# Kernel tuning notes

Measured on AMD Instinct MI355X. Metric: run time of the kernel, lower is better.

The kernel has to match this reference:

```python
import jax, jax.numpy as jnp
import numpy as np

N, E, D_IN, H, DH = 50000, 800000, 128, 4, 32
NEG_SLOPE = 0.01  # torch nn.LeakyReLU() default
EPS = 1e-16       # torch_geometric softmax epsilon


def setup_inputs() -> dict:
    key = jax.random.key(0)
    k0, k1, k2, k3, k4 = jax.random.split(key, 5)
    x = jax.random.normal(k0, (N, D_IN), dtype=jnp.float32)
    edge_index = jax.random.randint(k1, (2, E), 0, N, dtype=jnp.int64)
    # Glorot-uniform-ish scales
    s_proj = (6.0 / (D_IN + H * DH)) ** 0.5
    W_proj = jax.random.uniform(k2, (D_IN, H * DH), jnp.float32, -s_proj, s_proj)
    s_att = (6.0 / (H + 2 * DH)) ** 0.5
    att_w = jax.random.uniform(k3, (H, 2 * DH), jnp.float32, -s_att, s_att)
    W_skip = jax.random.uniform(k4, (D_IN, H * DH), jnp.float32, -s_proj, s_proj)
    return {"x": x, "W_proj": W_proj, "att_w": att_w, "W_skip": W_skip,
            "edge_index": edge_index}


def reference(x, W_proj, att_w, W_skip, edge_index):
    num_nodes = x.shape[0]
    h = (x @ W_proj).reshape(num_nodes, H, DH)          # [N,H,Dh]
    src, dst = edge_index[0], edge_index[1]
    h_src = h[src]                                      # [E,H,Dh] gather
    h_dst = h[dst]                                      # [E,H,Dh] gather
    # einsum('nah,nah->na', cat([h_src,h_dst],-1), a) == split-a form:
    a_src, a_dst = att_w[:, :DH], att_w[:, DH:]
    e = (jnp.einsum('ehd,hd->eh', h_src, a_src)
         + jnp.einsum('ehd,hd->eh', h_dst, a_dst))      # [E,H]
    e = jax.nn.leaky_relu(e, NEG_SLOPE)
    # segment softmax grouped by dst (max-stabilized, as in torch_geometric)
    e_max = jax.ops.segment_max(e, dst, num_segments=num_nodes)  # [N,H]
    e_exp = jnp.exp(e - e_max[dst])
    denom = jax.ops.segment_sum(e_exp, dst, num_segments=num_nodes)
    alpha = e_exp / (denom[dst] + EPS)                  # [E,H]
    # scatter-add aggregation (index_add_ by dst)
    h_prime = jax.ops.segment_sum(alpha[..., None] * h_src, dst,
                                  num_segments=num_nodes)  # [N,H,Dh]
    h_prime = h_prime + (x @ W_skip).reshape(num_nodes, H, DH)
    return h_prime.reshape(num_nodes, H * DH)
```

## Files before the change

kernel.cpp:

```cpp
#include <hip/hip_runtime.h>
#include <hip/hip_bf16.h>

#define N_NODES 50000
#define E_EDGES 800000
#define NHEAD 4
#define DHEAD 32
#define DOUT 128
#define NEG_SLOPE 0.01f
#define EPS_F 1e-16f
#define DMAX 256
#define ELP 264
#define NB 196
#define CAP 8192

typedef __attribute__((ext_vector_type(8))) short bf16x8;
typedef __attribute__((ext_vector_type(4))) float f32x4;

__device__ __forceinline__ float bf2f(unsigned short u) {
    return __uint_as_float((unsigned)u << 16);
}
__device__ __forceinline__ unsigned short f2bf(float f) {
    return __bfloat16_as_ushort(__float2bfloat16(f));
}

__device__ __forceinline__ void load_edge(const int* __restrict__ ei, int isI64,
                                          int e, int& src, int& dst) {
    if (isI64) { src = ei[2 * e]; dst = ei[2 * (E_EDGES + e)]; }
    else       { src = ei[e];     dst = ei[E_EDGES + e]; }
}

__global__ __launch_bounds__(128) void k_prep(const float* __restrict__ Wp,
                                              const float* __restrict__ Ws,
                                              const int* __restrict__ ei,
                                              unsigned short* __restrict__ Wt,
                                              int* __restrict__ flag) {
    int b = blockIdx.x;
    if (b < 256) {
        int c = b, k = threadIdx.x;
        float v = (c < DOUT) ? Wp[k * DOUT + c] : Ws[k * DOUT + (c - DOUT)];
        int nf = c >> 4, cl = c & 15;
        int ks = k >> 5, r = k & 31, lq = r >> 3, e = r & 7;
        Wt[(((nf * 4 + ks) << 6) + lq * 16 + cl) * 8 + e] = f2bf(v);
    } else {
        __shared__ int cnt;
        if (threadIdx.x == 0) cnt = 0;
        __syncthreads();
        int nz = 0;
        #pragma unroll
        for (int k2 = 0; k2 < 16; ++k2) {
            int pos = (threadIdx.x + k2 * 128) * 2 + 1;
            if (ei[pos] != 0) nz = 1;
        }
        if (nz) atomicOr(&cnt, 1);
        __syncthreads();
        if (threadIdx.x == 0) *flag = (cnt == 0) ? 1 : 0;
    }
}

#define HBP 136
#define SKP 132
__global__ __launch_bounds__(256) void k_gemm(const float* __restrict__ x,
                                              const unsigned short* __restrict__ Wt,
                                              const float* __restrict__ att,
                                              unsigned short* __restrict__ hb,
                                              float* __restrict__ as_,
                                              float* __restrict__ ad_,
                                              float* __restrict__ out) {
    __shared__ float SK[64 * SKP];
    __shared__ unsigned short HB[64 * HBP];
    char* XSc = (char*)SK;

    const int tid = threadIdx.x;
    const int rw  = tid >> 6;
    const int l   = tid & 63;
    const int l15 = l & 15;
    const int lq  = l >> 4;

    {
        int d = tid * 16;
        #pragma unroll
        for (int it = 0; it < 8; ++it, d += 4096) {
            int row = d >> 9, col = d & 511;
            int grow = blockIdx.x * 64 + row;
            if (grow > N_NODES - 1) grow = N_NODES - 1;
            float4 v = *(const float4*)((const char*)x + (size_t)grow * 512 + col);
            *(float4*)(XSc + (row << 9) + (col ^ ((row & 7) << 4))) = v;
        }
    }
    __syncthreads();

    const int rl = rw * 16 + l15;
    const int sw = (rl & 7) << 4;
    bf16x8 afr[4];
    #pragma unroll
    for (int ks = 0; ks < 4; ++ks) {
        int c0 = ks * 128 + lq * 32;
        float4 u0 = *(const float4*)(XSc + (rl << 9) + (c0 ^ sw));
        float4 u1 = *(const float4*)(XSc + (rl << 9) + ((c0 + 16) ^ sw));
        bf16x8 a;
        a[0] = (short)f2bf(u0.x); a[1] = (short)f2bf(u0.y);
        a[2] = (short)f2bf(u0.z); a[3] = (short)f2bf(u0.w);
        a[4] = (short)f2bf(u1.x); a[5] = (short)f2bf(u1.y);
        a[6] = (short)f2bf(u1.z); a[7] = (short)f2bf(u1.w);
        afr[ks] = a;
    }
    __syncthreads();

    f32x4 acc[16];
    #pragma unroll
    for (int nf = 0; nf < 16; ++nf) acc[nf] = (f32x4)(0.0f);

    #pragma unroll
    for (int nf = 0; nf < 16; ++nf) {
        #pragma unroll
        for (int ks = 0; ks < 4; ++ks) {
            bf16x8 b = *(const bf16x8*)(Wt + ((((nf * 4 + ks) << 6) + l) << 3));
            acc[nf] = __builtin_amdgcn_mfma_f32_16x16x32_bf16(afr[ks], b, acc[nf], 0, 0, 0);
        }
    }

    #pragma unroll
    for (int nf = 0; nf < 8; ++nf) {
        #pragma unroll
        for (int q = 0; q < 4; ++q) {
            int r2 = rw * 16 + lq * 4 + q;
            HB[r2 * HBP + nf * 16 + l15] = f2bf(acc[nf][q]);
        }
    }
    #pragma unroll
    for (int nf = 8; nf < 16; ++nf) {
        #pragma unroll
        for (int q = 0; q < 4; ++q) {
            int r2 = rw * 16 + lq * 4 + q;
            SK[r2 * SKP + (nf - 8) * 16 + l15] = acc[nf][q];
        }
    }
    __syncthreads();

    {
        int rl2 = tid >> 2, hd = tid & 3;
        const unsigned* HBu = (const unsigned*)HB;
        const float* a1 = att + hd * 2 * DHEAD;
        const float* a2 = a1 + DHEAD;
        float s1 = 0.0f, s2 = 0.0f;
        #pragma unroll
        for (int j = 0; j < 16; ++j) {
            unsigned u = HBu[rl2 * (HBP / 2) + hd * 16 + j];
            float lo = bf2f((unsigned short)(u & 0xffff));
            float hi = bf2f((unsigned short)(u >> 16));
            s1 += lo * a1[2 * j] + hi * a1[2 * j + 1];
            s2 += lo * a2[2 * j] + hi * a2[2 * j + 1];
        }
        int rowg = blockIdx.x * 64 + rl2;
        as_[(size_t)rowg * 4 + hd] = s1;
        ad_[(size_t)rowg * 4 + hd] = s2;
    }

    {
        const unsigned* HBu = (const unsigned*)HB;
        #pragma unroll
        for (int it = 0; it < 4; ++it) {
            int idx = it * 256 + tid;
            int row = idx >> 4, g = idx & 15;
            int wb = row * (HBP / 2) + g * 4;
            uint4 v;
            v.x = HBu[wb]; v.y = HBu[wb + 1]; v.z = HBu[wb + 2]; v.w = HBu[wb + 3];
            *(uint4*)(hb + ((size_t)(blockIdx.x * 64 + row)) * DOUT + g * 8) = v;
        }
    }
    {
        #pragma unroll
        for (int it = 0; it < 8; ++it) {
            int idx = it * 256 + tid;
            int row = idx >> 5, c4 = idx & 31;
            int rowg = blockIdx.x * 64 + row;
            if (rowg < N_NODES) {
                float4 v = *(const float4*)&SK[row * SKP + c4 * 4];
                *(float4*)(out + (size_t)rowg * DOUT + c4 * 4) = v;
            }
        }
    }
}

__global__ __launch_bounds__(256) void k_part(const int* __restrict__ ei,
                                              const int* __restrict__ flag,
                                              int* __restrict__ bucketCnt,
                                              unsigned* __restrict__ payload) {
    __shared__ int hist[NB];
    __shared__ int curs[NB];
    const int t = threadIdx.x;
    const int base = blockIdx.x * 3125;
    const int isI64 = *flag;

    for (int i = t; i < NB; i += 256) hist[i] = 0;
    __syncthreads();
    for (int i = t; i < 3125; i += 256) {
        int src, dst;
        load_edge(ei, isI64, base + i, src, dst);
        if ((unsigned)dst < N_NODES) atomicAdd(&hist[dst >> 8], 1);
    }
    __syncthreads();
    for (int i = t; i < NB; i += 256)
        curs[i] = atomicAdd(&bucketCnt[i], hist[i]);
    __syncthreads();
    for (int i = t; i < 3125; i += 256) {
        int src, dst;
        load_edge(ei, isI64, base + i, src, dst);
        if ((unsigned)src >= N_NODES || (unsigned)dst >= N_NODES) continue;
        int b = dst >> 8;
        int pos = atomicAdd(&curs[b], 1);
        if (pos < CAP)
            payload[((size_t)b << 13) + pos] = ((unsigned)(dst & 255) << 16) | (unsigned)src;
    }
}

__global__ __launch_bounds__(256) void k_csr(const int* __restrict__ bucketCnt,
                                             const unsigned* __restrict__ payload,
                                             int* __restrict__ deg,
                                             int* __restrict__ ofs,
                                             int* __restrict__ srcs) {
    __shared__ int h[256];
    __shared__ int cur[256];
    __shared__ int sc[256];
    const int b = blockIdx.x;
    const int t = threadIdx.x;
    int cnt = bucketCnt[b];
    if (cnt > CAP) cnt = CAP;
    const unsigned* __restrict__ pl = payload + ((size_t)b << 13);

    h[t] = 0;
    __syncthreads();
    for (int i = t; i < cnt; i += 256) atomicAdd(&h[pl[i] >> 16], 1);
    __syncthreads();
    int v = h[t];
    sc[t] = v;
    __syncthreads();
    #pragma unroll
    for (int off = 1; off < 256; off <<= 1) {
        int u = (t >= off) ? sc[t - off] : 0;
        __syncthreads();
        sc[t] += u;
        __syncthreads();
    }
    int ex = sc[t] - v;
    cur[t] = ex;
    int n = (b << 8) + t;
    if (n < N_NODES) { deg[n] = v; ofs[n] = (b << 13) + ex; }
    __syncthreads();
    for (int i = t; i < cnt; i += 256) {
        unsigned p = pl[i];
        int pos = atomicAdd(&cur[p >> 16], 1);
        srcs[((size_t)b << 13) + pos] = (int)(p & 0xFFFFu);
    }
}

__global__ __launch_bounds__(128) void k_gat(const int* __restrict__ ofs,
                                             const int* __restrict__ deg,
                                             const int* __restrict__ srcs,
                                             const float* __restrict__ as_,
                                             const float* __restrict__ ad_,
                                             const unsigned short* __restrict__ hb,
                                             float* __restrict__ out) {
    __shared__ float EL[2][NHEAD * ELP];
    __shared__ int   SRC[2][DMAX];

    const int sub = threadIdx.x >> 6;
    const int k   = threadIdx.x & 63;
    const int hd  = k >> 4;
    const int l16 = k & 15;
    const int n = blockIdx.x * 2 + sub;
    const int o = ofs[n];
    const int d = deg[n];
    const unsigned* __restrict__ hbu = (const unsigned*)hb;
    float* ELn = EL[sub];
    int*   SRCn = SRC[sub];

    int fast = __syncthreads_and(d <= DMAX);

    if (fast) {
        const float4 adv4 = *(const float4*)(ad_ + (size_t)n * 4);
        for (int e = k; e < d; e += 64) {
            int s = srcs[o + e];
            SRCn[e] = s;
            float4 a4 = *(const float4*)(as_ + (size_t)s * 4);
            float e0 = a4.x + adv4.x, e1 = a4.y + adv4.y;
            float e2 = a4.z + adv4.z, e3 = a4.w + adv4.w;
            ELn[0 * ELP + e] = (e0 > 0.0f) ? e0 : NEG_SLOPE * e0;
            ELn[1 * ELP + e] = (e1 > 0.0f) ? e1 : NEG_SLOPE * e1;
            ELn[2 * ELP + e] = (e2 > 0.0f) ? e2 : NEG_SLOPE * e2;
            ELn[3 * ELP + e] = (e3 > 0.0f) ? e3 : NEG_SLOPE * e3;
        }
        __syncthreads();
        float m = -3.4e38f;
        for (int i = l16; i < d; i += 16) m = fmaxf(m, ELn[hd * ELP + i]);
        #pragma unroll
        for (int off = 8; off; off >>= 1) m = fmaxf(m, __shfl_xor(m, off));
        float den = 0.0f;
        for (int i = l16; i < d; i += 16) {
            float p = __expf(ELn[hd * ELP + i] - m);
            ELn[hd * ELP + i] = p;
            den += p;
        }
        #pragma unroll
        for (int off = 8; off; off >>= 1) den += __shfl_xor(den, off);
        __syncthreads();
        float num0 = 0.0f, num1 = 0.0f;
        int i = 0;
        for (; i + 4 <= d; i += 4) {
            int s0 = SRCn[i], s1 = SRCn[i + 1], s2 = SRCn[i + 2], s3 = SRCn[i + 3];
            unsigned u0 = hbu[(size_t)s0 * (DOUT / 2) + k];
            unsigned u1 = hbu[(size_t)s1 * (DOUT / 2) + k];
            unsigned u2 = hbu[(size_t)s2 * (DOUT / 2) + k];
            unsigned u3 = hbu[(size_t)s3 * (DOUT / 2) + k];
            float p0 = ELn[hd * ELP + i];
            float p1 = ELn[hd * ELP + i + 1];
            float p2 = ELn[hd * ELP + i + 2];
            float p3 = ELn[hd * ELP + i + 3];
            num0 = fmaf(p0, bf2f((unsigned short)(u0 & 0xffff)), num0);
            num1 = fmaf(p0, bf2f((unsigned short)(u0 >> 16)), num1);
            num0 = fmaf(p1, bf2f((unsigned short)(u1 & 0xffff)), num0);
            num1 = fmaf(p1, bf2f((unsigned short)(u1 >> 16)), num1);
            num0 = fmaf(p2, bf2f((unsigned short)(u2 & 0xffff)), num0);
            num1 = fmaf(p2, bf2f((unsigned short)(u2 >> 16)), num1);
            num0 = fmaf(p3, bf2f((unsigned short)(u3 & 0xffff)), num0);
            num1 = fmaf(p3, bf2f((unsigned short)(u3 >> 16)), num1);
        }
        for (; i < d; ++i) {
            float p = ELn[hd * ELP + i];
            int s = SRCn[i];
            unsigned u = hbu[(size_t)s * (DOUT / 2) + k];
            num0 = fmaf(p, bf2f((unsigned short)(u & 0xffff)), num0);
            num1 = fmaf(p, bf2f((unsigned short)(u >> 16)), num1);
        }
        float inv = 1.0f / (den + EPS_F);
        float2* op = (float2*)(out + (size_t)n * DOUT + 2 * k);
        float2 sk = *op;
        *op = make_float2(num0 * inv + sk.x, num1 * inv + sk.y);
    } else {
        const float adv = ad_[(size_t)n * 4 + hd];
        float m = -3.4e38f;
        for (int i = 0; i < d; ++i) {
            float el = as_[(size_t)srcs[o + i] * 4 + hd] + adv;
            el = (el > 0.0f) ? el : NEG_SLOPE * el;
            m = fmaxf(m, el);
        }
        float den = 0.0f, num0 = 0.0f, num1 = 0.0f;
        for (int i = 0; i < d; ++i) {
            int s = srcs[o + i];
            float el = as_[(size_t)s * 4 + hd] + adv;
            el = (el > 0.0f) ? el : NEG_SLOPE * el;
            float p = __expf(el - m);
            den += p;
            unsigned u = hbu[(size_t)s * (DOUT / 2) + k];
            num0 = fmaf(p, bf2f((unsigned short)(u & 0xffff)), num0);
            num1 = fmaf(p, bf2f((unsigned short)(u >> 16)), num1);
        }
        float inv = 1.0f / (den + EPS_F);
        float2* op = (float2*)(out + (size_t)n * DOUT + 2 * k);
        float2 sk = *op;
        *op = make_float2(num0 * inv + sk.x, num1 * inv + sk.y);
    }
}

extern "C" void kernel_launch(void* const* d_in, const int* in_sizes, int n_in,
                              void* d_out, int out_size, void* d_ws, size_t ws_size,
                              hipStream_t stream) {
    const float* x   = (const float*)d_in[0];
    const float* Wp  = (const float*)d_in[1];
    const float* att = (const float*)d_in[2];
    const float* Ws  = (const float*)d_in[3];
    const int*   ei  = (const int*)d_in[4];
    float* out = (float*)d_out;

    char* ws = (char*)d_ws;
    unsigned short* hb        = (unsigned short*)(ws);
    unsigned short* Wt        = (unsigned short*)(ws + 12812288);
    float*          as_       = (float*)(ws + 12877824);
    float*          ad_       = (float*)(ws + 13678592);
    int*            deg       = (int*)(ws + 14479360);
    int*            ofs       = (int*)(ws + 14680064);
    unsigned*       payload   = (unsigned*)(ws + 14880768);
    int*            srcs      = (int*)(ws + 21303296);
    int*            bucketCnt = (int*)(ws + 27725824);
    int*            flag      = (int*)(ws + 27726848);

    hipMemsetAsync(bucketCnt, 0, NB * 4, stream);

    k_prep<<<257, 128, 0, stream>>>(Wp, Ws, ei, Wt, flag);
    k_gemm<<<(N_NODES + 63) / 64, 256, 0, stream>>>(x, Wt, att, hb, as_, ad_, out);
    k_part<<<256, 256, 0, stream>>>(ei, flag, bucketCnt, payload);
    k_csr<<<NB, 256, 0, stream>>>(bucketCnt, payload, deg, ofs, srcs);
    k_gat<<<N_NODES / 2, 128, 0, stream>>>(ofs, deg, srcs, as_, ad_, hb, out);
}
```

Measured before the change: 118.2 us.

## Merge edge partition into GEMM launch and store GEMM outputs directly from registers

The edge bucketing kernel and the projection GEMM now run as one launch: the first 256 blocks do the partition and the rest do the GEMM, so the two independent stages can overlap and one launch is removed. The GEMM converts x to bf16 while staging it into shared memory and swaps the MFMA operand order so each lane holds a row's outputs. The attention dot products are then computed straight from the accumulators with shuffle reductions, and hb and out are written directly without a shared-memory round trip. This trades fewer barriers and less shared-memory traffic for scattered 8-byte and 16-byte global stores and a mixed-workload grid.

```diff
diff --git a/kernel.cpp b/kernel.cpp
--- a/kernel.cpp
+++ b/kernel.cpp
@@ -12,6 +12,7 @@
 #define ELP 264
 #define NB 196
 #define CAP 8192
+#define XSP 136
 
 typedef __attribute__((ext_vector_type(8))) short bf16x8;
 typedef __attribute__((ext_vector_type(4))) float f32x4;
@@ -57,54 +58,76 @@
     }
 }
 
-#define HBP 136
-#define SKP 132
-__global__ __launch_bounds__(256) void k_gemm(const float* __restrict__ x,
-                                              const unsigned short* __restrict__ Wt,
-                                              const float* __restrict__ att,
-                                              unsigned short* __restrict__ hb,
-                                              float* __restrict__ as_,
-                                              float* __restrict__ ad_,
-                                              float* __restrict__ out) {
-    __shared__ float SK[64 * SKP];
-    __shared__ unsigned short HB[64 * HBP];
-    char* XSc = (char*)SK;
-
+__global__ __launch_bounds__(256) void k_gemm_part(const float* __restrict__ x,
+                                                   const unsigned short* __restrict__ Wt,
+                                                   const float* __restrict__ att,
+                                                   const int* __restrict__ ei,
+                                                   const int* __restrict__ flag,
+                                                   int* __restrict__ bucketCnt,
+                                                   unsigned* __restrict__ payload,
+                                                   unsigned short* __restrict__ hb,
+                                                   float* __restrict__ as_,
+                                                   float* __restrict__ ad_,
+                                                   float* __restrict__ out) {
+    __shared__ __align__(16) char BUF[64 * XSP * 2];
     const int tid = threadIdx.x;
+
+    if (blockIdx.x < 256) {
+        int* hist = (int*)BUF;
+        int* curs = hist + NB;
+        const int base = blockIdx.x * 3125;
+        const int isI64 = *flag;
+
+        for (int i = tid; i < NB; i += 256) hist[i] = 0;
+        __syncthreads();
+        for (int i = tid; i < 3125; i += 256) {
+            int src, dst;
+            load_edge(ei, isI64, base + i, src, dst);
+            if ((unsigned)dst < N_NODES) atomicAdd(&hist[dst >> 8], 1);
+        }
+        __syncthreads();
+        for (int i = tid; i < NB; i += 256)
+            curs[i] = atomicAdd(&bucketCnt[i], hist[i]);
+        __syncthreads();
+        for (int i = tid; i < 3125; i += 256) {
+            int src, dst;
+            load_edge(ei, isI64, base + i, src, dst);
+            if ((unsigned)src >= N_NODES || (unsigned)dst >= N_NODES) continue;
+            int b = dst >> 8;
+            int pos = atomicAdd(&curs[b], 1);
+            if (pos < CAP)
+                payload[((size_t)b << 13) + pos] = ((unsigned)(dst & 255) << 16) | (unsigned)src;
+        }
+        return;
+    }
+
+    unsigned short* XSB = (unsigned short*)BUF;
+    const int gb  = blockIdx.x - 256;
     const int rw  = tid >> 6;
     const int l   = tid & 63;
     const int l15 = l & 15;
     const int lq  = l >> 4;
+    const int rowbase = gb * 64 + rw * 16;
 
     {
-        int d = tid * 16;
-        #pragma unroll
-        for (int it = 0; it < 8; ++it, d += 4096) {
-            int row = d >> 9, col = d & 511;
-            int grow = blockIdx.x * 64 + row;
+        #pragma unroll
+        for (int it = 0; it < 8; ++it) {
+            int e = it * 1024 + tid * 4;
+            int row = e >> 7, col = e & 127;
+            int grow = gb * 64 + row;
             if (grow > N_NODES - 1) grow = N_NODES - 1;
-            float4 v = *(const float4*)((const char*)x + (size_t)grow * 512 + col);
-            *(float4*)(XSc + (row << 9) + (col ^ ((row & 7) << 4))) = v;
-        }
-    }
-    __syncthreads();
-
-    const int rl = rw * 16 + l15;
-    const int sw = (rl & 7) << 4;
-    bf16x8 afr[4];
-    #pragma unroll
-    for (int ks = 0; ks < 4; ++ks) {
-        int c0 = ks * 128 + lq * 32;
-        float4 u0 = *(const float4*)(XSc + (rl << 9) + (c0 ^ sw));
-        float4 u1 = *(const float4*)(XSc + (rl << 9) + ((c0 + 16) ^ sw));
-        bf16x8 a;
-        a[0] = (short)f2bf(u0.x); a[1] = (short)f2bf(u0.y);
-        a[2] = (short)f2bf(u0.z); a[3] = (short)f2bf(u0.w);
-        a[4] = (short)f2bf(u1.x); a[5] = (short)f2bf(u1.y);
-        a[6] = (short)f2bf(u1.z); a[7] = (short)f2bf(u1.w);
-        afr[ks] = a;
-    }
-    __syncthreads();
+            float4 v = *(const float4*)(x + (size_t)grow * DOUT + col);
+            ushort4 pk = make_ushort4(f2bf(v.x), f2bf(v.y), f2bf(v.z), f2bf(v.w));
+            *(ushort4*)(XSB + row * XSP + col) = pk;
+        }
+    }
+    __syncthreads();
+
+    bf16x8 xfr[4];
+    const char* xrow = (const char*)XSB + (rw * 16 + l15) * (XSP * 2);
+    #pragma unroll
+    for (int ks = 0; ks < 4; ++ks)
+        xfr[ks] = *(const bf16x8*)(xrow + ks * 64 + lq * 16);
 
     f32x4 acc[16];
     #pragma unroll
@@ -114,103 +137,44 @@
     for (int nf = 0; nf < 16; ++nf) {
         #pragma unroll
         for (int ks = 0; ks < 4; ++ks) {
-            bf16x8 b = *(const bf16x8*)(Wt + ((((nf * 4 + ks) << 6) + l) << 3));
-            acc[nf] = __builtin_amdgcn_mfma_f32_16x16x32_bf16(afr[ks], b, acc[nf], 0, 0, 0);
-        }
-    }
-
+            bf16x8 w = *(const bf16x8*)(Wt + ((((nf * 4 + ks) << 6) + l) << 3));
+            acc[nf] = __builtin_amdgcn_mfma_f32_16x16x32_bf16(w, xfr[ks], acc[nf], 0, 0, 0);
+        }
+    }
+
+    const int r = rowbase + l15;
+    float ps1[4] = {0.f, 0.f, 0.f, 0.f}, ps2[4] = {0.f, 0.f, 0.f, 0.f};
     #pragma unroll
     for (int nf = 0; nf < 8; ++nf) {
-        #pragma unroll
-        for (int q = 0; q < 4; ++q) {
-            int r2 = rw * 16 + lq * 4 + q;
-            HB[r2 * HBP + nf * 16 + l15] = f2bf(acc[nf][q]);
-        }
-    }
-    #pragma unroll
-    for (int nf = 8; nf < 16; ++nf) {
-        #pragma unroll
-        for (int q = 0; q < 4; ++q) {
-            int r2 = rw * 16 + lq * 4 + q;
-            SK[r2 * SKP + (nf - 8) * 16 + l15] = acc[nf][q];
-        }
-    }
-    __syncthreads();
-
-    {
-        int rl2 = tid >> 2, hd = tid & 3;
-        const unsigned* HBu = (const unsigned*)HB;
-        const float* a1 = att + hd * 2 * DHEAD;
-        const float* a2 = a1 + DHEAD;
-        float s1 = 0.0f, s2 = 0.0f;
-        #pragma unroll
-        for (int j = 0; j < 16; ++j) {
-            unsigned u = HBu[rl2 * (HBP / 2) + hd * 16 + j];
-            float lo = bf2f((unsigned short)(u & 0xffff));
-            float hi = bf2f((unsigned short)(u >> 16));
-            s1 += lo * a1[2 * j] + hi * a1[2 * j + 1];
-            s2 += lo * a2[2 * j] + hi * a2[2 * j + 1];
-        }
-        int rowg = blockIdx.x * 64 + rl2;
-        as_[(size_t)rowg * 4 + hd] = s1;
-        ad_[(size_t)rowg * 4 + hd] = s2;
-    }
-
-    {
-        const unsigned* HBu = (const unsigned*)HB;
-        #pragma unroll
-        for (int it = 0; it < 4; ++it) {
-            int idx = it * 256 + tid;
-            int row = idx >> 4, g = idx & 15;
-            int wb = row * (HBP / 2) + g * 4;
-            uint4 v;
-            v.x = HBu[wb]; v.y = HBu[wb + 1]; v.z = HBu[wb + 2]; v.w = HBu[wb + 3];
-            *(uint4*)(hb + ((size_t)(blockIdx.x * 64 + row)) * DOUT + g * 8) = v;
-        }
-    }
-    {
-        #pragma unroll
-        for (int it = 0; it < 8; ++it) {
-            int idx = it * 256 + tid;
-            int row = idx >> 5, c4 = idx & 31;
-            int rowg = blockIdx.x * 64 + row;
-            if (rowg < N_NODES) {
-                float4 v = *(const float4*)&SK[row * SKP + c4 * 4];
-                *(float4*)(out + (size_t)rowg * DOUT + c4 * 4) = v;
-            }
-        }
-    }
-}
-
-__global__ __launch_bounds__(256) void k_part(const int* __restrict__ ei,
-                                              const int* __restrict__ flag,
-                                              int* __restrict__ bucketCnt,
-                                              unsigned* __restrict__ payload) {
-    __shared__ int hist[NB];
-    __shared__ int curs[NB];
-    const int t = threadIdx.x;
-    const int base = blockIdx.x * 3125;
-    const int isI64 = *flag;
-
-    for (int i = t; i < NB; i += 256) hist[i] = 0;
-    __syncthreads();
-    for (int i = t; i < 3125; i += 256) {
-        int src, dst;
-        load_edge(ei, isI64, base + i, src, dst);
-        if ((unsigned)dst < N_NODES) atomicAdd(&hist[dst >> 8], 1);
-    }
-    __syncthreads();
-    for (int i = t; i < NB; i += 256)
-        curs[i] = atomicAdd(&bucketCnt[i], hist[i]);
-    __syncthreads();
-    for (int i = t; i < 3125; i += 256) {
-        int src, dst;
-        load_edge(ei, isI64, base + i, src, dst);
-        if ((unsigned)src >= N_NODES || (unsigned)dst >= N_NODES) continue;
-        int b = dst >> 8;
-        int pos = atomicAdd(&curs[b], 1);
-        if (pos < CAP)
-            payload[((size_t)b << 13) + pos] = ((unsigned)(dst & 255) << 16) | (unsigned)src;
+        int hd = nf >> 1;
+        int jb = (nf & 1) * 16 + lq * 4;
+        float4 w1 = *(const float4*)(att + hd * 2 * DHEAD + jb);
+        float4 w2 = *(const float4*)(att + hd * 2 * DHEAD + DHEAD + jb);
+        f32x4 v = acc[nf];
+        ps1[hd] += v[0] * w1.x + v[1] * w1.y + v[2] * w1.z + v[3] * w1.w;
+        ps2[hd] += v[0] * w2.x + v[1] * w2.y + v[2] * w2.z + v[3] * w2.w;
+        ushort4 pk = make_ushort4(f2bf(v[0]), f2bf(v[1]), f2bf(v[2]), f2bf(v[3]));
+        *(ushort4*)(hb + (size_t)r * DOUT + nf * 16 + lq * 4) = pk;
+    }
+    #pragma unroll
+    for (int hd = 0; hd < 4; ++hd) {
+        ps1[hd] += __shfl_xor(ps1[hd], 16); ps1[hd] += __shfl_xor(ps1[hd], 32);
+        ps2[hd] += __shfl_xor(ps2[hd], 16); ps2[hd] += __shfl_xor(ps2[hd], 32);
+    }
+    if (lq == 0) {
+        #pragma unroll
+        for (int hd = 0; hd < 4; ++hd) {
+            as_[(size_t)r * 4 + hd] = ps1[hd];
+            ad_[(size_t)r * 4 + hd] = ps2[hd];
+        }
+    }
+    if (r < N_NODES) {
+        #pragma unroll
+        for (int nf = 8; nf < 16; ++nf) {
+            f32x4 v = acc[nf];
+            *(float4*)(out + (size_t)r * DOUT + (nf - 8) * 16 + lq * 4) =
+                make_float4(v[0], v[1], v[2], v[3]);
+        }
     }
 }
 
@@ -387,8 +351,8 @@
     hipMemsetAsync(bucketCnt, 0, NB * 4, stream);
 
     k_prep<<<257, 128, 0, stream>>>(Wp, Ws, ei, Wt, flag);
-    k_gemm<<<(N_NODES + 63) / 64, 256, 0, stream>>>(x, Wt, att, hb, as_, ad_, out);
-    k_part<<<256, 256, 0, stream>>>(ei, flag, bucketCnt, payload);
+    k_gemm_part<<<256 + (N_NODES + 63) / 64, 256, 0, stream>>>(
+        x, Wt, att, ei, flag, bucketCnt, payload, hb, as_, ad_, out);
     k_csr<<<NB, 256, 0, stream>>>(bucketCnt, payload, deg, ofs, srcs);
     k_gat<<<N_NODES / 2, 128, 0, stream>>>(ofs, deg, srcs, as_, ad_, hb, out);
 }
```

New measurement: 111.4 us. 5.7% less time.
